# Kernel optimization log

Hardware: AMD Instinct MI355X
Metric: run time of the kernel (lower is better)

Reference implementation:

```python
import jax, jax.numpy as jnp
import numpy as np

NUM_HEADS = 8
ATTN_C = 8
EPS = 1e-5


def setup_inputs() -> dict:
    key = jax.random.key(0)
    ks = jax.random.split(key, 8)
    B, S, R, C = 1, 2048, 384, 64
    H, c = NUM_HEADS, ATTN_C
    sc = 1.0 / np.sqrt(C)
    return {
        "x1d": jax.random.normal(ks[0], (B, S, R, C), dtype=jnp.float32),
        "ln_w": jnp.ones((C,), jnp.float32),
        "ln_b": jnp.zeros((C,), jnp.float32),
        "Wq": jax.random.normal(ks[1], (C, H * c), jnp.float32) * sc,
        "Wk": jax.random.normal(ks[2], (C, c), jnp.float32) * sc,
        "Wv": jax.random.normal(ks[3], (C, c), jnp.float32) * sc,
        "Wg": jax.random.normal(ks[4], (C, H * c), jnp.float32) * sc,
        "bg": jnp.zeros((H * c,), jnp.float32),
        "Wf": jax.random.normal(ks[5], (H * c, C), jnpp := jnp.float32) * sc,
        "bf": jnp.zeros((C,), jnp.float32),
    }


def reference(x1d, ln_w, ln_b, Wq, Wk, Wv, Wg, bg, Wf, bf):
    H, c = NUM_HEADS, ATTN_C
    # swap seq/res axes: [B, S, R, C] -> [B, R, S, C]; attention runs over S (MSA column)
    x = jnp.swapaxes(x1d, -2, -3)
    mu = jnp.mean(x, axis=-1, keepdims=True)
    var = jnp.mean(jnp.square(x - mu), axis=-1, keepdims=True)
    xn = (x - mu) / jnp.sqrt(var + EPS) * ln_w + ln_b
    B, R, S, C = xn.shape
    # mean-pooled query over the sequence axis
    q_avg = jnp.mean(xn, axis=-2)                                  # [B, R, C]
    q = (q_avg @ Wq).reshape(B, R, H, c) * (c ** -0.5)             # [B, R, H, c]
    k = xn @ Wk                                                    # [B, R, S, c] (single shared head)
    v = xn @ Wv                                                    # [B, R, S, c]
    gate = jax.nn.sigmoid((xn @ Wg + bg).reshape(B, R, S, H, c))   # [B, R, S, H, c]
    w = jax.nn.softmax(jnp.einsum('brhc,brsc->brhs', q, k), axis=-1)  # [B, R, H, S]
    o = jnp.einsum('brhs,brsc->brhc', w, v)                        # [B, R, H, c]
    out = (o[:, :, None, :, :] * gate).reshape(B, R, S, H * c)     # broadcast over S, gated
    out = out @ Wf + bf                                            # [B, R, S, C]
    return jnp.swapaxes(out, -2, -3)                               # [B, S, R, C]
```

## Files before the change

### kernel.cpp

```cpp
#include <hip/hip_runtime.h>

#define SEQ  2048
#define RDIM 384
#define CDIM 64

typedef __attribute__((ext_vector_type(8))) short s16x8;
typedef __attribute__((ext_vector_type(4))) float f32x4;
#define MFMA(a,b,c) __builtin_amdgcn_mfma_f32_16x16x32_bf16(a,b,c,0,0,0)

__device__ __forceinline__ unsigned short f2bf(float x) {
    union { float f; unsigned u; } a; a.f = x;
    unsigned r = a.u + 0x7fffu + ((a.u >> 16) & 1u);
    return (unsigned short)(r >> 16);
}
__device__ __forceinline__ unsigned pack2(float lo, float hi) {
    return (unsigned)f2bf(lo) | ((unsigned)f2bf(hi) << 16);
}
__device__ __forceinline__ float bf2f(unsigned u16) {
    union { unsigned u; float f; } a; a.u = u16 << 16; return a.f;
}
__device__ __forceinline__ float uaf(unsigned u) {
    union { unsigned u; float f; } a; a.u = u; return a.f;
}

#define SWZ(row,k) ((row)*64 + (((((k)>>3) ^ ((row)&7)))<<3) + ((k)&7))

__global__ __launch_bounds__(256) void k_prep(
    const float* __restrict__ Wk, const float* __restrict__ Wv,
    const float* __restrict__ Wg, const float* __restrict__ Wf,
    const float* __restrict__ lnw, const float* __restrict__ lnb,
    const float* __restrict__ bg,
    unsigned short* __restrict__ wkvt, unsigned short* __restrict__ wgt,
    unsigned short* __restrict__ wfp, float* __restrict__ kvbias,
    float* __restrict__ bgp)
{
    const int t = threadIdx.x, b = blockIdx.x;
    if (b == 0) {
        for (int idx = t; idx < 16 * 64; idx += 256) {
            const int kc = idx >> 6, k = idx & 63;
            const float v = lnw[k] * ((kc < 8) ? Wk[k * 8 + kc] : Wv[k * 8 + (kc - 8)]);
            wkvt[SWZ(kc, k)] = f2bf(v);
        }
        if (t < 16) {
            float a = 0.f;
            for (int k = 0; k < 64; k++)
                a += lnb[k] * ((t < 8) ? Wk[k * 8 + t] : Wv[k * 8 + (t - 8)]);
            kvbias[t] = a;
        }
    } else if (b == 1) {
        for (int idx = t; idx < 64 * 64; idx += 256) {
            const int col = idx >> 6, k = idx & 63;
            wgt[SWZ(col, k)] = f2bf(lnw[k] * Wg[k * 64 + col]);
        }
        if (t < 64) {
            float a = bg[t];
            for (int k = 0; k < 64; k++) a += lnb[k] * Wg[k * 64 + t];
            bgp[t] = a;
        }
    } else {
        for (int idx = t; idx < 64 * 64; idx += 256) {
            const int cout = idx >> 6, p = idx & 63;
            const int kst = p >> 5, h = (p >> 3) & 3, rr = p & 7;
            const int j = kst * 32 + (rr < 4 ? 4 * h + rr : 16 + 4 * h + (rr - 4));
            wfp[SWZ(cout, p)] = f2bf(Wf[j * 64 + cout]);
        }
    }
}

__global__ __launch_bounds__(256) void k_phase1(
    const float* __restrict__ x, const unsigned short* __restrict__ wkvt,
    float* __restrict__ qpart, unsigned short* __restrict__ kv)
{
    __shared__ __align__(16) unsigned short xs[128 * 64];
    __shared__ __align__(16) unsigned short wkv[16 * 64];
    const int t = threadIdx.x;
    ((unsigned*)wkv)[t]       = ((const unsigned*)wkvt)[t];
    ((unsigned*)wkv)[t + 256] = ((const unsigned*)wkvt)[t + 256];

    const int rtile  = blockIdx.x % 24;
    const int schunk = blockIdx.x / 24;
    const int g  = t >> 4;
    const int c4 = t & 15;
    const int r = rtile * 16 + g;
    const int wv = t >> 6, lane = t & 63, hi = lane >> 4, l15 = lane & 15;

    float qs0 = 0.f, qs1 = 0.f, qs2 = 0.f, qs3 = 0.f;
    for (int sub = 0; sub < 8; ++sub) {
        __syncthreads();
        #pragma unroll
        for (int it = 0; it < 8; ++it) {
            const int row = it * 16 + g;
            const int s = schunk * 64 + sub * 8 + it;
            const float4 xv = *(const float4*)(x + ((size_t)s * RDIM + r) * CDIM + (c4 << 2));
            float sum = xv.x + xv.y + xv.z + xv.w;
            float sq  = xv.x * xv.x + xv.y * xv.y + xv.z * xv.z + xv.w * xv.w;
            #pragma unroll
            for (int m = 1; m < 16; m <<= 1) {
                sum += __shfl_xor(sum, m, 16);
                sq  += __shfl_xor(sq,  m, 16);
            }
            const float mu   = sum * (1.0f / 64.0f);
            const float rstd = rsqrtf(sq * (1.0f / 64.0f) - mu * mu + 1e-5f);
            const float xn0 = (xv.x - mu) * rstd;
            const float xn1 = (xv.y - mu) * rstd;
            const float xn2 = (xv.z - mu) * rstd;
            const float xn3 = (xv.w - mu) * rstd;
            qs0 += xn0; qs1 += xn1; qs2 += xn2; qs3 += xn3;
            ushort4 pk; pk.x = f2bf(xn0); pk.y = f2bf(xn1); pk.z = f2bf(xn2); pk.w = f2bf(xn3);
            *(ushort4*)&xs[row * 64 + ((((c4 >> 1) ^ (row & 7)) << 3) | ((c4 & 1) << 2))] = pk;
        }
        __syncthreads();
        f32x4 acc0 = 0, acc1 = 0;
        #pragma unroll
        for (int kst = 0; kst < 2; ++kst) {
            const int kg = (kst * 4 + hi);
            const s16x8 a = *(const s16x8*)&wkv[l15 * 64 + ((kg ^ (l15 & 7)) << 3)];
            const int row0 = wv * 32 + l15;
            const s16x8 b0 = *(const s16x8*)&xs[row0 * 64 + ((kg ^ (l15 & 7)) << 3)];
            const s16x8 b1 = *(const s16x8*)&xs[(row0 + 16) * 64 + ((kg ^ (l15 & 7)) << 3)];
            acc0 = MFMA(a, b0, acc0);
            acc1 = MFMA(a, b1, acc1);
        }
        #pragma unroll
        for (int ni = 0; ni < 2; ++ni) {
            const f32x4 av = ni ? acc1 : acc0;
            const int srow = schunk * 64 + sub * 8 + 2 * wv + ni;
            const int rrow = rtile * 16 + l15;
            ushort4 pk; pk.x = f2bf(av[0]); pk.y = f2bf(av[1]); pk.z = f2bf(av[2]); pk.w = f2bf(av[3]);
            *(ushort4*)(kv + ((size_t)rrow * SEQ + srow) * 16 + (hi << 2)) = pk;
        }
    }
    float4 q4; q4.x = qs0; q4.y = qs1; q4.z = qs2; q4.w = qs3;
    *(float4*)(qpart + ((size_t)schunk * RDIM + r) * CDIM + (c4 << 2)) = q4;
}

__global__ __launch_bounds__(256) void k_phase2a(
    const float* __restrict__ qpart, const float* __restrict__ Wq,
    const float* __restrict__ lnw, const float* __restrict__ lnb,
    const float* __restrict__ kvbias, const unsigned short* __restrict__ kv,
    float* __restrict__ num, float* __restrict__ den)
{
    __shared__ float qa[64];
    __shared__ float ql[64];
    __shared__ float lbias[8];
    __shared__ float hredd[4][8];
    __shared__ float wred[4][64];
    const int t = threadIdx.x;
    const int r = blockIdx.x >> 1;
    const int half = blockIdx.x & 1;
    if (t < 64) {
        float ssum = 0.f;
        #pragma unroll
        for (int ch = 0; ch < 32; ch++) ssum += qpart[(size_t)ch * (RDIM * CDIM) + r * 64 + t];
        qa[t] = ssum;
    }
    __syncthreads();
    if (t < 64) {
        float a = 0.f;
        for (int i = 0; i < 64; i++)
            a += (qa[i] * (1.0f / 2048.0f) * lnw[i] + lnb[i]) * Wq[i * 64 + t];
        ql[t] = a * 0.35355339059327373f;
    }
    __syncthreads();
    if (t < 8) {
        float a = 0.f;
        #pragma unroll
        for (int c = 0; c < 8; c++) a += ql[t * 8 + c] * kvbias[c];
        lbias[t] = a;
    }
    __syncthreads();

    const unsigned short* kvr = kv + (size_t)r * (SEQ * 16);
    float acc[64];
    float pd[8];
    #pragma unroll
    for (int j = 0; j < 64; j++) acc[j] = 0.f;
    #pragma unroll
    for (int h = 0; h < 8; h++) pd[h] = 0.f;

    #pragma unroll
    for (int i = 0; i < 4; i++) {
        const int s = half * 1024 + i * 256 + t;
        const uint4 ku = *(const uint4*)(kvr + (size_t)s * 16);
        const uint4 vu = *(const uint4*)(kvr + (size_t)s * 16 + 8);
        float kf[8], vf[8];
        kf[0] = bf2f(ku.x & 0xffff); kf[1] = bf2f(ku.x >> 16);
        kf[2] = bf2f(ku.y & 0xffff); kf[3] = bf2f(ku.y >> 16);
        kf[4] = bf2f(ku.z & 0xffff); kf[5] = bf2f(ku.z >> 16);
        kf[6] = bf2f(ku.w & 0xffff); kf[7] = bf2f(ku.w >> 16);
        vf[0] = bf2f(vu.x & 0xffff); vf[1] = bf2f(vu.x >> 16);
        vf[2] = bf2f(vu.y & 0xffff); vf[3] = bf2f(vu.y >> 16);
        vf[4] = bf2f(vu.z & 0xffff); vf[5] = bf2f(vu.z >> 16);
        vf[6] = bf2f(vu.w & 0xffff); vf[7] = bf2f(vu.w >> 16);
        #pragma unroll
        for (int h = 0; h < 8; h++) {
            float a = lbias[h];
            #pragma unroll
            for (int c = 0; c < 8; c++) a += ql[h * 8 + c] * kf[c];
            const float e = __expf(a);
            pd[h] += e;
            #pragma unroll
            for (int c = 0; c < 8; c++) acc[h * 8 + c] += e * vf[c];
        }
    }
    #pragma unroll
    for (int m = 1; m < 64; m <<= 1) {
        #pragma unroll
        for (int j = 0; j < 64; j++) acc[j] += __shfl_xor(acc[j], m, 64);
        #pragma unroll
        for (int h = 0; h < 8; h++) pd[h] += __shfl_xor(pd[h], m, 64);
    }
    const int wvi = t >> 6, lane = t & 63;
    if (lane == 0) {
        #pragma unroll
        for (int j = 0; j < 64; j++) wred[wvi][j] = acc[j];
        #pragma unroll
        for (int h = 0; h < 8; h++) hredd[wvi][h] = pd[h];
    }
    __syncthreads();
    if (t < 64)
        num[(size_t)(half * RDIM + r) * 64 + t] = wred[0][t] + wred[1][t] + wred[2][t] + wred[3][t];
    if (t < 8)
        den[(size_t)(half * RDIM + r) * 8 + t] = hredd[0][t] + hredd[1][t] + hredd[2][t] + hredd[3][t];
}

__global__ __launch_bounds__(256) void k_phase2b(
    const float* __restrict__ num, const float* __restrict__ den,
    const float* __restrict__ kvbias, unsigned short* __restrict__ ofimg)
{
    const int idx = blockIdx.x * 256 + threadIdx.x;
    const int r = idx >> 6, c = idx & 63;
    const float n = num[idx] + num[RDIM * 64 + idx];
    const float d = den[r * 8 + (c >> 3)] + den[(RDIM + r) * 8 + (c >> 3)];
    const float o = n / d + kvbias[8 + (c & 7)];
    const int rt = r >> 7, row = r & 127;
    const int wv = row >> 5, ni = (row >> 4) & 1, l15 = row & 15;
    const int mi = c >> 4, hi = (c >> 2) & 3, rg = c & 3;
    const int tt = wv * 64 + hi * 16 + l15;
    const int slot = ni * 16 + mi * 4 + rg;
    ofimg[((rt * 256 + tt) << 5) + slot] = f2bf(o);
}

__global__ __launch_bounds__(256, 3) void k_phase3(
    const float* __restrict__ x,
    const unsigned short* __restrict__ wgt, const unsigned short* __restrict__ wfp,
    const float* __restrict__ bgp, const float* __restrict__ bf_,
    const unsigned short* __restrict__ ofimg, float* __restrict__ out)
{
    __shared__ __align__(16) unsigned short xs[2][128 * 64];
    __shared__ __align__(16) unsigned short wg[64 * 64];
    __shared__ __align__(16) unsigned short wf[64 * 64];
    const int t = threadIdx.x;
    const int rt = blockIdx.x % 3;
    const int sb = blockIdx.x / 3;
    const int rbase = rt * 128;

    #pragma unroll
    for (int i = 0; i < 8; ++i) ((unsigned*)wg)[t + i * 256] = ((const unsigned*)wgt)[t + i * 256];
    #pragma unroll
    for (int i = 0; i < 8; ++i) ((unsigned*)wf)[t + i * 256] = ((const unsigned*)wfp)[t + i * 256];

    const int wv = t >> 6, lane = t & 63, hi = lane >> 4, l15 = lane & 15;

    unsigned opk[16];
    {
        const unsigned* osrc = (const unsigned*)ofimg + (size_t)(rt * 256 + t) * 16;
        #pragma unroll
        for (int i = 0; i < 16; ++i) opk[i] = osrc[i];
    }
    float bgf[4][4], bff[4][4];
    #pragma unroll
    for (int mi = 0; mi < 4; ++mi) *(float4*)bgf[mi] = *(const float4*)(bgp + mi * 16 + hi * 4);
    #pragma unroll
    for (int ci = 0; ci < 4; ++ci) *(float4*)bff[ci] = *(const float4*)(bf_ + ci * 16 + hi * 4);

    const int li = t & 3, p = t >> 2;
    float4 xv[2][4];
    {
        const int s0 = sb * 8;
        #pragma unroll
        for (int k = 0; k < 2; ++k) {
            const float* xp = x + ((size_t)s0 * RDIM + rbase + k * 64 + p) * CDIM + li * 16;
            #pragma unroll
            for (int j = 0; j < 4; ++j) xv[k][j] = *(const float4*)(xp + j * 4);
        }
    }

    for (int si = 0; si < 8; ++si) {
        const int s = sb * 8 + si;
        unsigned short* xb = xs[si & 1];
        #pragma unroll
        for (int k = 0; k < 2; ++k) {
            const int row = k * 64 + p;
            float sum = 0.f, sq = 0.f;
            #pragma unroll
            for (int j = 0; j < 4; ++j) {
                sum += xv[k][j].x + xv[k][j].y + xv[k][j].z + xv[k][j].w;
                sq  += xv[k][j].x * xv[k][j].x + xv[k][j].y * xv[k][j].y
                     + xv[k][j].z * xv[k][j].z + xv[k][j].w * xv[k][j].w;
            }
            sum += __shfl_xor(sum, 1, 4); sum += __shfl_xor(sum, 2, 4);
            sq  += __shfl_xor(sq,  1, 4); sq  += __shfl_xor(sq,  2, 4);
            const float mu   = sum * (1.0f / 64.0f);
            const float rstd = rsqrtf(sq * (1.0f / 64.0f) - mu * mu + 1e-5f);
            uint4 w0, w1;
            w0.x = pack2((xv[k][0].x - mu) * rstd, (xv[k][0].y - mu) * rstd);
            w0.y = pack2((xv[k][0].z - mu) * rstd, (xv[k][0].w - mu) * rstd);
            w0.z = pack2((xv[k][1].x - mu) * rstd, (xv[k][1].y - mu) * rstd);
            w0.w = pack2((xv[k][1].z - mu) * rstd, (xv[k][1].w - mu) * rstd);
            w1.x = pack2((xv[k][2].x - mu) * rstd, (xv[k][2].y - mu) * rstd);
            w1.y = pack2((xv[k][2].z - mu) * rstd, (xv[k][2].w - mu) * rstd);
            w1.z = pack2((xv[k][3].x - mu) * rstd, (xv[k][3].y - mu) * rstd);
            w1.w = pack2((xv[k][3].z - mu) * rstd, (xv[k][3].w - mu) * rstd);
            *(uint4*)&xb[row * 64 + (((2 * li)     ^ (row & 7)) << 3)] = w0;
            *(uint4*)&xb[row * 64 + (((2 * li + 1) ^ (row & 7)) << 3)] = w1;
        }
        if (si < 7) {
            const int sn = s + 1;
            #pragma unroll
            for (int k = 0; k < 2; ++k) {
                const float* xp = x + ((size_t)sn * RDIM + rbase + k * 64 + p) * CDIM + li * 16;
                #pragma unroll
                for (int j = 0; j < 4; ++j) xv[k][j] = *(const float4*)(xp + j * 4);
            }
        }
        asm volatile("s_waitcnt lgkmcnt(0)" ::: "memory");
        __builtin_amdgcn_s_barrier();
        asm volatile("" ::: "memory");

        f32x4 acc1[4][2];
        #pragma unroll
        for (int mi = 0; mi < 4; ++mi) { acc1[mi][0] = 0; acc1[mi][1] = 0; }
        #pragma unroll
        for (int kst = 0; kst < 2; ++kst) {
            const int swz = (((kst * 4 + hi) ^ (l15 & 7)) << 3);
            const s16x8 bfr0 = *(const s16x8*)&xb[(wv * 32 + l15) * 64 + swz];
            const s16x8 bfr1 = *(const s16x8*)&xb[(wv * 32 + 16 + l15) * 64 + swz];
            #pragma unroll
            for (int mi = 0; mi < 4; ++mi) {
                const s16x8 afr = *(const s16x8*)&wg[(mi * 16 + l15) * 64 + swz];
                acc1[mi][0] = MFMA(afr, bfr0, acc1[mi][0]);
                acc1[mi][1] = MFMA(afr, bfr1, acc1[mi][1]);
            }
        }
        s16x8 a2[2][2];
        #pragma unroll
        for (int ni = 0; ni < 2; ++ni) {
            #pragma unroll
            for (int mi = 0; mi < 4; ++mi) {
                #pragma unroll
                for (int rg = 0; rg < 4; ++rg) {
                    const int slot = ni * 16 + mi * 4 + rg;
                    const unsigned u = opk[slot >> 1];
                    const float of = uaf((slot & 1) ? (u & 0xffff0000u) : (u << 16));
                    const float z = acc1[mi][ni][rg] + bgf[mi][rg];
                    const float tv = of / (1.0f + __expf(-z));
                    a2[ni][mi >> 1][((mi & 1) << 2) + rg] = (short)f2bf(tv);
                }
            }
        }
        f32x4 acc2[2][4];
        #pragma unroll
        for (int ni = 0; ni < 2; ++ni)
            #pragma unroll
            for (int ci = 0; ci < 4; ++ci) acc2[ni][ci] = 0;
        #pragma unroll
        for (int kst = 0; kst < 2; ++kst) {
            const int swz = (((kst * 4 + hi) ^ (l15 & 7)) << 3);
            #pragma unroll
            for (int ci = 0; ci < 4; ++ci) {
                const s16x8 wffr = *(const s16x8*)&wf[(ci * 16 + l15) * 64 + swz];
                acc2[0][ci] = MFMA(wffr, a2[0][kst], acc2[0][ci]);
                acc2[1][ci] = MFMA(wffr, a2[1][kst], acc2[1][ci]);
            }
        }
        #pragma unroll
        for (int ni = 0; ni < 2; ++ni) {
            float* op = out + ((size_t)s * RDIM + rbase + wv * 32 + ni * 16 + l15) * 64 + hi * 4;
            #pragma unroll
            for (int ci = 0; ci < 4; ++ci) {
                float4 res;
                res.x = acc2[ni][ci][0] + bff[ci][0];
                res.y = acc2[ni][ci][1] + bff[ci][1];
                res.z = acc2[ni][ci][2] + bff[ci][2];
                res.w = acc2[ni][ci][3] + bff[ci][3];
                *(float4*)(op + ci * 16) = res;
            }
        }
    }
}

extern "C" void kernel_launch(void* const* d_in, const int* in_sizes, int n_in,
                              void* d_out, int out_size, void* d_ws, size_t ws_size,
                              hipStream_t stream)
{
    const float* x   = (const float*)d_in[0];
    const float* lnw = (const float*)d_in[1];
    const float* lnb = (const float*)d_in[2];
    const float* Wq  = (const float*)d_in[3];
    const float* Wk  = (const float*)d_in[4];
    const float* Wv  = (const float*)d_in[5];
    const float* Wg  = (const float*)d_in[6];
    const float* bg  = (const float*)d_in[7];
    const float* Wf  = (const float*)d_in[8];
    const float* bf  = (const float*)d_in[9];

    char* ws = (char*)d_ws;
    float*          qpart  = (float*)ws;
    unsigned short* kv     = (unsigned short*)(ws + 3145728);
    float*          num    = (float*)(ws + 28311552);
    float*          den    = (float*)(ws + 28508160);
    unsigned short* ofimg  = (unsigned short*)(ws + 28532736);
    unsigned short* wkvt   = (unsigned short*)(ws + 28581888);
    unsigned short* wgt    = (unsigned short*)(ws + 28583936);
    unsigned short* wfp    = (unsigned short*)(ws + 28592128);
    float*          kvbias = (float*)(ws + 28600320);
    float*          bgp    = (float*)(ws + 28600384);

    float* outp = (float*)d_out;

    k_prep<<<3, 256, 0, stream>>>(Wk, Wv, Wg, Wf, lnw, lnb, bg, wkvt, wgt, wfp, kvbias, bgp);
    k_phase1<<<768, 256, 0, stream>>>(x, wkvt, qpart, kv);
    k_phase2a<<<768, 256, 0, stream>>>(qpart, Wq, lnw, lnb, kvbias, kv, num, den);
    k_phase2b<<<96, 256, 0, stream>>>(num, den, kvbias, ofimg);
    k_phase3<<<768, 256, 0, stream>>>(x, wgt, wfp, bgp, bf, ofimg, outp);
}
```

Measured before the change: 171.6 us.

## Stage kv tile in LDS for coalesced stores; split gated output into hi/lo bf16

Phase 1 now writes its K/V projections into a shared-memory tile and then copies each row's contiguous 1024-element segment to global memory with 16-byte stores, replacing scattered 8-byte stores. Separately, phase 2b keeps the attention output in fp32, and phase 3 splits the gated activation into high and low bf16 parts and issues two MFMAs per step for the output projection. The second part raises precision at the cost of doubling the output-projection MFMAs and of a larger fp32 output buffer, and the new LDS tile increases phase 1's shared-memory use.

```diff
diff --git a/kernel.cpp b/kernel.cpp
--- a/kernel.cpp
+++ b/kernel.cpp
@@ -19,11 +19,10 @@
 __device__ __forceinline__ float bf2f(unsigned u16) {
     union { unsigned u; float f; } a; a.u = u16 << 16; return a.f;
 }
-__device__ __forceinline__ float uaf(unsigned u) {
-    union { unsigned u; float f; } a; a.u = u; return a.f;
-}
 
 #define SWZ(row,k) ((row)*64 + (((((k)>>3) ^ ((row)&7)))<<3) + ((k)&7))
+
+#define KVS_STRIDE 1032
 
 __global__ __launch_bounds__(256) void k_prep(
     const float* __restrict__ Wk, const float* __restrict__ Wv,
@@ -73,6 +72,7 @@
 {
     __shared__ __align__(16) unsigned short xs[128 * 64];
     __shared__ __align__(16) unsigned short wkv[16 * 64];
+    __shared__ __align__(16) unsigned short kvs[16 * KVS_STRIDE];
     const int t = threadIdx.x;
     ((unsigned*)wkv)[t]       = ((const unsigned*)wkvt)[t];
     ((unsigned*)wkv)[t + 256] = ((const unsigned*)wkvt)[t + 256];
@@ -124,14 +124,22 @@
         #pragma unroll
         for (int ni = 0; ni < 2; ++ni) {
             const f32x4 av = ni ? acc1 : acc0;
-            const int srow = schunk * 64 + sub * 8 + 2 * wv + ni;
-            const int rrow = rtile * 16 + l15;
+            const int sloc = sub * 8 + 2 * wv + ni;
             ushort4 pk; pk.x = f2bf(av[0]); pk.y = f2bf(av[1]); pk.z = f2bf(av[2]); pk.w = f2bf(av[3]);
-            *(ushort4*)(kv + ((size_t)rrow * SEQ + srow) * 16 + (hi << 2)) = pk;
+            *(ushort4*)&kvs[l15 * KVS_STRIDE + sloc * 16 + (hi << 2)] = pk;
         }
     }
     float4 q4; q4.x = qs0; q4.y = qs1; q4.z = qs2; q4.w = qs3;
     *(float4*)(qpart + ((size_t)schunk * RDIM + r) * CDIM + (c4 << 2)) = q4;
+
+    __syncthreads();
+    {
+        const int rr = t >> 4, seg = t & 15;
+        uint4* dstq = (uint4*)(kv + (size_t)(rtile * 16 + rr) * (SEQ * 16) + (size_t)schunk * 1024);
+        #pragma unroll
+        for (int i = 0; i < 8; ++i)
+            dstq[seg + 16 * i] = *(const uint4*)&kvs[rr * KVS_STRIDE + (seg + 16 * i) * 8];
+    }
 }
 
 __global__ __launch_bounds__(256) void k_phase2a(
@@ -226,7 +234,7 @@
 
 __global__ __launch_bounds__(256) void k_phase2b(
     const float* __restrict__ num, const float* __restrict__ den,
-    const float* __restrict__ kvbias, unsigned short* __restrict__ ofimg)
+    const float* __restrict__ kvbias, float* __restrict__ ofimg)
 {
     const int idx = blockIdx.x * 256 + threadIdx.x;
     const int r = idx >> 6, c = idx & 63;
@@ -238,14 +246,14 @@
     const int mi = c >> 4, hi = (c >> 2) & 3, rg = c & 3;
     const int tt = wv * 64 + hi * 16 + l15;
     const int slot = ni * 16 + mi * 4 + rg;
-    ofimg[((rt * 256 + tt) << 5) + slot] = f2bf(o);
+    ofimg[((rt * 256 + tt) << 5) + slot] = o;
 }
 
 __global__ __launch_bounds__(256, 3) void k_phase3(
     const float* __restrict__ x,
     const unsigned short* __restrict__ wgt, const unsigned short* __restrict__ wfp,
     const float* __restrict__ bgp, const float* __restrict__ bf_,
-    const unsigned short* __restrict__ ofimg, float* __restrict__ out)
+    const float* __restrict__ ofimg, float* __restrict__ out)
 {
     __shared__ __align__(16) unsigned short xs[2][128 * 64];
     __shared__ __align__(16) unsigned short wg[64 * 64];
@@ -262,11 +270,11 @@
 
     const int wv = t >> 6, lane = t & 63, hi = lane >> 4, l15 = lane & 15;
 
-    unsigned opk[16];
+    float of32[32];
     {
-        const unsigned* osrc = (const unsigned*)ofimg + (size_t)(rt * 256 + t) * 16;
-        #pragma unroll
-        for (int i = 0; i < 16; ++i) opk[i] = osrc[i];
+        const float* osrc = ofimg + (size_t)(rt * 256 + t) * 32;
+        #pragma unroll
+        for (int i = 0; i < 8; ++i) *(float4*)&of32[i * 4] = *(const float4*)(osrc + i * 4);
     }
     float bgf[4][4], bff[4][4];
     #pragma unroll
@@ -343,7 +351,7 @@
                 acc1[mi][1] = MFMA(afr, bfr1, acc1[mi][1]);
             }
         }
-        s16x8 a2[2][2];
+        s16x8 a2h[2][2], a2l[2][2];
         #pragma unroll
         for (int ni = 0; ni < 2; ++ni) {
             #pragma unroll
@@ -351,11 +359,12 @@
                 #pragma unroll
                 for (int rg = 0; rg < 4; ++rg) {
                     const int slot = ni * 16 + mi * 4 + rg;
-                    const unsigned u = opk[slot >> 1];
-                    const float of = uaf((slot & 1) ? (u & 0xffff0000u) : (u << 16));
                     const float z = acc1[mi][ni][rg] + bgf[mi][rg];
-                    const float tv = of / (1.0f + __expf(-z));
-                    a2[ni][mi >> 1][((mi & 1) << 2) + rg] = (short)f2bf(tv);
+                    const float tv = of32[slot] / (1.0f + __expf(-z));
+                    const unsigned short hb = f2bf(tv);
+                    const float lo = tv - bf2f(hb);
+                    a2h[ni][mi >> 1][((mi & 1) << 2) + rg] = (short)hb;
+                    a2l[ni][mi >> 1][((mi & 1) << 2) + rg] = (short)f2bf(lo);
                 }
             }
         }
@@ -370,8 +379,10 @@
             #pragma unroll
             for (int ci = 0; ci < 4; ++ci) {
                 const s16x8 wffr = *(const s16x8*)&wf[(ci * 16 + l15) * 64 + swz];
-                acc2[0][ci] = MFMA(wffr, a2[0][kst], acc2[0][ci]);
-                acc2[1][ci] = MFMA(wffr, a2[1][kst], acc2[1][ci]);
+                acc2[0][ci] = MFMA(wffr, a2h[0][kst], acc2[0][ci]);
+                acc2[0][ci] = MFMA(wffr, a2l[0][kst], acc2[0][ci]);
+                acc2[1][ci] = MFMA(wffr, a2h[1][kst], acc2[1][ci]);
+                acc2[1][ci] = MFMA(wffr, a2l[1][kst], acc2[1][ci]);
             }
         }
         #pragma unroll
@@ -410,12 +421,12 @@
     unsigned short* kv     = (unsigned short*)(ws + 3145728);
     float*          num    = (float*)(ws + 28311552);
     float*          den    = (float*)(ws + 28508160);
-    unsigned short* ofimg  = (unsigned short*)(ws + 28532736);
-    unsigned short* wkvt   = (unsigned short*)(ws + 28581888);
-    unsigned short* wgt    = (unsigned short*)(ws + 28583936);
-    unsigned short* wfp    = (unsigned short*)(ws + 28592128);
-    float*          kvbias = (float*)(ws + 28600320);
-    float*          bgp    = (float*)(ws + 28600384);
+    float*          ofimg  = (float*)(ws + 28532736);
+    unsigned short* wkvt   = (unsigned short*)(ws + 28631040);
+    unsigned short* wgt    = (unsigned short*)(ws + 28633088);
+    unsigned short* wfp    = (unsigned short*)(ws + 28641280);
+    float*          kvbias = (float*)(ws + 28649472);
+    float*          bgp    = (float*)(ws + 28649536);
 
     float* outp = (float*)d_out;
 
```

Result: slower. 196.7 us (+14.6%).
